# Kernel optimization log

Measured on AMD Instinct MI355X. Metric: run time of the kernel, lower is better.

The kernel has to match this reference:

```python
import jax, jax.numpy as jnp
import numpy as np

N, E, G = 50000, 500000, 512
IN_C, HID, EXTRA = 6, 32, 4
EPS = 1e-5


def setup_inputs() -> dict:
    key = jax.random.key(0)
    ks = jax.random.split(key, 24)
    rn = lambda k, s, sc=0.1: jax.random.normal(k, s, jnp.float32) * sc
    return {
        "x": jax.random.normal(ks[0], (N, IN_C), jnp.float32),
        "edge_index": jax.random.randint(ks[1], (2, E), 0, N),
        "edge_attr": jax.random.normal(ks[2], (E, 5), jnp.float32),
        "batch": jnp.sort(jax.random.randint(ks[3], (N,), 0, G)),
        "graph_attr": jax.random.normal(ks[4], (G, EXTRA), jnp.float32),
        # edge MLP 1: 5 -> 32 -> IN_C*HID
        "e1_w1": rn(ks[5], (5, 32)), "e1_b1": jnp.zeros((32,), jnp.float32),
        "e1_w2": rn(ks[6], (32, IN_C * HID)), "e1_b2": jnp.zeros((IN_C * HID,), jnp.float32),
        "root1": rn(ks[7], (IN_C, HID)), "bias1": jnp.zeros((HID,), jnp.float32),
        "bn1_g": jnp.ones((HID,), jnp.float32), "bn1_b": jnp.zeros((HID,), jnp.float32),
        # edge MLP 2: 5 -> 32 -> HID*HID
        "e2_w1": rn(ks[8], (5, 32)), "e2_b1": jnp.zeros((32,), jnp.float32),
        "e2_w2": rn(ks[9], (32, HID * HID)), "e2_b2": jnp.zeros((HID * HID,), jnp.float32),
        "root2": rn(ks[10], (HID, HID)), "bias2": jnp.zeros((HID,), jnp.float32),
        "bn2_g": jnp.ones((HID,), jnp.float32), "bn2_b": jnp.zeros((HID,), jnp.float32),
        "fc_w": rn(ks[11], (HID + EXTRA, 3)), "fc_b": jnp.zeros((3,), jnp.float32),
    }


def _nnconv(x, src, dst, edge_attr, w1, b1, w2, b2, root, bias, in_c, out_c):
    # per-edge weight matrix from edge MLP
    h = jax.nn.relu(edge_attr @ w1 + b1)                    # [E, 32]
    W = (h @ w2 + b2).reshape(-1, in_c, out_c)              # [E, in_c, out_c]
    msg = jnp.einsum('ei,eio->eo', x[src], W)               # per-edge matvec
    agg = jax.ops.segment_sum(msg, dst, num_segments=N)
    cnt = jax.ops.segment_sum(jnp.ones((msg.shape[0],), msg.dtype), dst, num_segments=N)
    agg = agg / jnp.maximum(cnt, 1.0)[:, None]              # scatter-mean
    return agg + x @ root + bias


def _bn(x, g, b):
    mu = jnp.mean(x, axis=0)
    var = jnp.mean(jnp.square(x - mu), axis=0)
    return (x - mu) * jax.lax.rsqrt(var + EPS) * g + b


def reference(x, edge_index, edge_attr, batch, graph_attr,
              e1_w1, e1_b1, e1_w2, e1_b2, root1, bias1, bn1_g, bn1_b,
              e2_w1, e2_b1, e2_w2, e2_b2, root2, bias2, bn2_g, bn2_b,
              fc_w, fc_b):
    src, dst = edge_index[0], edge_index[1]
    h = _nnconv(x, src, dst, edge_attr, e1_w1, e1_b1, e1_w2, e1_b2, root1, bias1, IN_C, HID)
    h = jax.nn.relu(_bn(h, bn1_g, bn1_b))  # dropout = identity (eval)
    h = _nnconv(h, src, dst, edge_attr, e2_w1, e2_b1, e2_w2, e2_b2, root2, bias2, HID, HID)
    h = jax.nn.relu(_bn(h, bn2_g, bn2_b))
    # global mean pool over graphs
    psum = jax.ops.segment_sum(h, batch, num_segments=G)
    pcnt = jax.ops.segment_sum(jnp.ones((N,), h.dtype), batch, num_segments=G)
    pooled = psum / jnp.maximum(pcnt, 1.0)[:, None]
    combined = jnp.concatenate([pooled, graph_attr], axis=1)  # [G, HID+EXTRA]
    return combined @ fc_w + fc_b                              # [G, 3]
```

## Files before the change

### kernel.cpp

```cpp
#include <hip/hip_runtime.h>

#define NN 50000
#define EE 500000
#define GG 512

typedef _Float16 f16x8 __attribute__((ext_vector_type(8)));
typedef _Float16 f16x2 __attribute__((ext_vector_type(2)));
typedef float f32x16 __attribute__((ext_vector_type(16)));

union F16x8U { f16x8 v8; f16x2 v2[4]; unsigned u[4]; };

__device__ __forceinline__ unsigned splat_h(float a){
  return __builtin_bit_cast(unsigned, __builtin_amdgcn_cvt_pkrtz(a, a));
}

__device__ __forceinline__ void gload16(const _Float16* g, _Float16* l){
  __builtin_amdgcn_global_load_lds(
      (const __attribute__((address_space(1))) unsigned int*)g,
      (__attribute__((address_space(3))) unsigned int*)l, 16, 0, 0);
}

#define NL1 (20*512)
#define NL2 (72*512)
__launch_bounds__(256)
__global__ void prep_k(const float* __restrict__ x,
                       const float* __restrict__ w2a, const float* __restrict__ b2a,
                       const float* __restrict__ w2b, const float* __restrict__ b2b,
                       _Float16* __restrict__ xh, _Float16* __restrict__ BtL1,
                       _Float16* __restrict__ BtL2)
{
  int idx = blockIdx.x*256 + threadIdx.x;
  if (idx < NL1){
    int t = idx >> 9, r = idx & 511;
    int lane = r >> 3, j = r & 7;
    int col = lane & 31, hi = lane >> 5;
    int ki = 16*t + 8*hi + j;
    int k = ki >> 3, i = ki & 7;
    float v = 0.f;
    if (i < 6){
      if (k < 32)       v = w2a[k*192 + i*32 + col];
      else if (k == 32) v = b2a[i*32 + col];
    }
    BtL1[idx] = (_Float16)v;
  } else if (idx < NL1 + NL2){
    int q = idx - NL1;
    int t = q >> 9, r = q & 511;
    int lane = r >> 3, j = r & 7;
    int col = lane & 31, hi = lane >> 5;
    int ki = 16*t + 8*hi + j;
    int k = ki >> 5, i = ki & 31;
    float v = 0.f;
    if (k < 32)       v = w2b[k*1024 + i*32 + col];
    else if (k == 32) v = b2b[i*32 + col];
    BtL2[q] = (_Float16)v;
  } else {
    int j = idx - (NL1 + NL2);
    if (j < NN*8){
      int n = j >> 3, i = j & 7;
      xh[j] = (_Float16)((i < 6) ? x[n*6 + i] : 0.f);
    }
  }
}

__launch_bounds__(256)
__global__ void hist_k(const int* __restrict__ ei, int* __restrict__ hist)
{
  int e = blockIdx.x*256 + threadIdx.x;
  if (e < EE) atomicAdd(&hist[ei[EE + e]], 1);
}

__launch_bounds__(256)
__global__ void scan1_k(const int* __restrict__ hist, int* __restrict__ part,
                        int* __restrict__ blk)
{
  __shared__ int s[256];
  int t = threadIdx.x, b = blockIdx.x, i = b*256 + t;
  int v = (i < NN) ? hist[i] : 0;
  s[t] = v; __syncthreads();
  #pragma unroll
  for (int off = 1; off < 256; off <<= 1){
    int u = (t >= off) ? s[t-off] : 0;
    __syncthreads();
    s[t] += u;
    __syncthreads();
  }
  if (i < NN) part[i] = s[t] - v;
  if (t == 255) blk[b] = s[255];
}

__launch_bounds__(256)
__global__ void scan2_k(int* __restrict__ blk, int nblk)
{
  __shared__ int s[256];
  int t = threadIdx.x;
  int v = (t < nblk) ? blk[t] : 0;
  s[t] = v; __syncthreads();
  #pragma unroll
  for (int off = 1; off < 256; off <<= 1){
    int u = (t >= off) ? s[t-off] : 0;
    __syncthreads();
    s[t] += u;
    __syncthreads();
  }
  if (t < nblk) blk[t] = s[t] - v;
}

__launch_bounds__(256)
__global__ void rowptr_k(const int* __restrict__ part, const int* __restrict__ blk,
                         int* __restrict__ rowptr)
{
  int n = blockIdx.x*256 + threadIdx.x;
  if (n < NN) rowptr[n] = part[n] + blk[n >> 8];
}

__launch_bounds__(256)
__global__ void scatter_k(const int* __restrict__ ei, const float* __restrict__ ea,
                          const int* __restrict__ rowptr, int* __restrict__ cursor,
                          int* __restrict__ esrc, int* __restrict__ edst,
                          float* __restrict__ eap)
{
  int e = blockIdx.x*256 + threadIdx.x;
  if (e < EE){
    int d = ei[EE + e];
    int slot = rowptr[d] + atomicAdd(&cursor[d], 1);
    esrc[slot] = ei[e];
    edst[slot] = d;
    #pragma unroll
    for (int q = 0; q < 5; ++q) eap[(long)slot*5 + q] = ea[(long)e*5 + q];
  }
}

template<int CONV>
__launch_bounds__(512, 4)
__global__ void conv_msg_k(const _Float16* __restrict__ xh,
                           const int* __restrict__ esrc,
                           const int* __restrict__ edst,
                           const float* __restrict__ eap,
                           const float* __restrict__ w1,
                           const float* __restrict__ b1,
                           const _Float16* __restrict__ Btg,
                           const int* __restrict__ rowptr,
                           const int* __restrict__ deg,
                           float* __restrict__ agg)
{
  constexpr int BTB_F16 = (CONV == 1) ? 10240 : 8192;
  __shared__ unsigned hs2[256][37];
  __shared__ _Float16 btb[BTB_F16];
  __shared__ int segrow[258];
  __shared__ int segcnt[4];

  const int tid  = threadIdx.x;
  const int lane = tid & 63;
  const int wave = tid >> 6;
  const int e0   = blockIdx.x * 256;
  const int nvalid = (EE - e0 < 256) ? (EE - e0) : 256;

  if (CONV == 1){
    #pragma unroll
    for (int i = 0; i < 3; ++i){
      int s = wave + 8*i;
      if (s < 20) gload16(Btg + (long)s*512 + lane*8, btb + s*512);
    }
  } else {
    gload16(Btg + (long)wave*512 + lane*8, btb + wave*512);
  }

  {
    int e  = tid >> 1;
    int kb = (tid & 1) * 16;
    int eg = e0 + e;
    bool valid = eg < EE;
    float eav[5];
    #pragma unroll
    for (int q = 0; q < 5; ++q) eav[q] = valid ? eap[(long)eg*5 + q] : 0.f;
    #pragma unroll
    for (int k = kb; k < kb + 16; ++k){
      float a = b1[k];
      #pragma unroll
      for (int q = 0; q < 5; ++q) a += eav[q] * w1[q*32 + k];
      hs2[e][k] = splat_h(fmaxf(a, 0.f));
    }
    if (kb == 16){
      hs2[e][32] = splat_h(1.f);
      hs2[e][33] = 0u; hs2[e][34] = 0u; hs2[e][35] = 0u;
    }
  }
  __syncthreads();

  const int col = lane & 31;
  const int hi  = lane >> 5;
  const int el  = wave*32 + col;
  const int emy = e0 + el;
  const int src = (emy < EE) ? esrc[emy] : 0;

  F16x8U xa, xb;
  if (CONV == 1){
    xa.v8 = *(const f16x8*)(xh + (long)src*8);
    xb.v8 = xa.v8;
  } else {
    xa.v8 = *(const f16x8*)(xh + (long)src*32 + 8*hi);
    xb.v8 = *(const f16x8*)(xh + (long)src*32 + 16 + 8*hi);
  }

  unsigned h2[(CONV == 1) ? 17 : 33];
  if (CONV == 1){
    #pragma unroll
    for (int t = 0; t < 17; ++t) h2[t] = hs2[el][2*t + hi];
  } else {
    #pragma unroll
    for (int kk = 0; kk < 33; ++kk) h2[kk] = hs2[el][kk];
  }

  f32x16 acc;
  #pragma unroll
  for (int r = 0; r < 16; ++r) acc[r] = 0.f;

  if (CONV == 1){
    #pragma unroll
    for (int t = 0; t < 17; ++t){
      f16x8 bf = *(const f16x8*)&btb[t*512 + lane*8];
      f16x2 hv = __builtin_bit_cast(f16x2, h2[t]);
      F16x8U af;
      #pragma unroll
      for (int p = 0; p < 4; ++p) af.v2[p] = hv * xa.v2[p];
      acc = __builtin_amdgcn_mfma_f32_32x32x16_f16(af.v8, bf, acc, 0, 0, 0);
    }
    __syncthreads();
  } else {
    #pragma unroll
    for (int c = 0; c < 9; ++c){
      if (c < 8){
        gload16(Btg + (long)((c+1)*8 + wave)*512 + lane*8,
                btb + ((c+1)&1)*4096 + wave*512);
      }
      const int tmax = (c == 8) ? 2 : 8;
      #pragma unroll
      for (int tt = 0; tt < tmax; ++tt){
        const int t = c*8 + tt;
        f16x8 bf = *(const f16x8*)&btb[(c&1)*4096 + tt*512 + lane*8];
        f16x2 hv = __builtin_bit_cast(f16x2, h2[t >> 1]);
        const F16x8U& xs = (t & 1) ? xb : xa;
        F16x8U af;
        #pragma unroll
        for (int p = 0; p < 4; ++p) af.v2[p] = hv * xs.v2[p];
        acc = __builtin_amdgcn_mfma_f32_32x32x16_f16(af.v8, bf, acc, 0, 0, 0);
      }
      __syncthreads();
    }
  }

  float* msg = (float*)&hs2[0][0];

  #pragma unroll
  for (int g = 0; g < 4; ++g){
    #pragma unroll
    for (int r = 0; r < 4; ++r){
      int row = wave*32 + r + 8*g + 4*hi;
      msg[row*37 + col] = acc[4*g + r];
    }
  }

  bool st = false;
  if (tid < 256){
    int eg = e0 + tid;
    st = (tid < nvalid) && (tid == 0 || edst[eg] != edst[eg-1]);
  }
  unsigned long long m = __ballot(st);
  int rank = __popcll(m & ((1ull << lane) - 1ull));
  if (tid < 256 && lane == 0) segcnt[wave] = (int)__popcll(m);
  __syncthreads();
  int nseg = segcnt[0] + segcnt[1] + segcnt[2] + segcnt[3];
  if (st){
    int off = 0;
    #pragma unroll
    for (int w = 0; w < 3; ++w) if (w < wave) off += segcnt[w];
    segrow[rank + off] = tid;
  }
  if (tid == 256) segrow[nseg] = nvalid;
  __syncthreads();

  const int c2 = tid & 31;
  for (int s = tid >> 5; s < nseg; s += 16){
    int r0 = segrow[s], r1 = segrow[s+1];
    float sum = 0.f;
    for (int r = r0; r < r1; ++r) sum += msg[r*37 + c2];
    int d  = edst[e0 + r0];
    int rp = rowptr[d];
    if (rp >= e0 && rp + deg[d] <= e0 + nvalid)
      agg[(long)d*32 + c2] = sum;
    else
      atomicAdd(&agg[(long)d*32 + c2], sum);
  }
}

template<int IN_C>
__launch_bounds__(256)
__global__ void node_update_k(const float* __restrict__ xin, const float* __restrict__ root,
                              const float* __restrict__ bias, const int* __restrict__ cnt,
                              float* __restrict__ buf, float* __restrict__ stats, int N)
{
  __shared__ float rs[IN_C*32];
  __shared__ float bs[32];
  __shared__ float redS[4][32], redQ[4][32];
  int tid = threadIdx.x;
  for (int i = tid; i < IN_C*32; i += 256) rs[i] = root[i];
  if (tid < 32) bs[tid] = bias[tid];
  __syncthreads();
  int o = tid & 31, slot = tid >> 5;
  float s = 0.f, q = 0.f;
  for (int n = blockIdx.x*8 + slot; n < N; n += gridDim.x*8){
    float c = fmaxf((float)cnt[n], 1.f);
    float v = buf[(long)n*32 + o] / c + bs[o];
    if constexpr (IN_C == 32){
      const float4* xr = (const float4*)&xin[(long)n*32];
      #pragma unroll
      for (int i4 = 0; i4 < 8; ++i4){
        float4 xv = xr[i4];
        v += xv.x*rs[(i4*4+0)*32+o] + xv.y*rs[(i4*4+1)*32+o]
           + xv.z*rs[(i4*4+2)*32+o] + xv.w*rs[(i4*4+3)*32+o];
      }
    } else {
      const float2* xr = (const float2*)&xin[(long)n*6];
      #pragma unroll
      for (int i2 = 0; i2 < 3; ++i2){
        float2 xv = xr[i2];
        v += xv.x*rs[(i2*2+0)*32+o] + xv.y*rs[(i2*2+1)*32+o];
      }
    }
    buf[(long)n*32 + o] = v;
    s += v; q += v*v;
  }
  s += __shfl_xor(s, 32); q += __shfl_xor(q, 32);
  int wv = tid >> 6;
  if ((tid & 63) < 32){ redS[wv][o] = s; redQ[wv][o] = q; }
  __syncthreads();
  if (tid < 32){
    float ts = 0.f, tq = 0.f;
    #pragma unroll
    for (int w = 0; w < 4; ++w){ ts += redS[w][tid]; tq += redQ[w][tid]; }
    atomicAdd(&stats[tid], ts); atomicAdd(&stats[32 + tid], tq);
  }
}

__launch_bounds__(256)
__global__ void bn_relu_k(float* __restrict__ buf, _Float16* __restrict__ bufh,
                          const float* __restrict__ stats,
                          const float* __restrict__ gg, const float* __restrict__ bb,
                          float invN, int total)
{
  int i = blockIdx.x*256 + threadIdx.x;
  if (i < total){
    int o = i & 31;
    float mu  = stats[o] * invN;
    float var = stats[32+o] * invN - mu*mu;
    float v = fmaxf((buf[i] - mu) * rsqrtf(var + 1e-5f) * gg[o] + bb[o], 0.f);
    buf[i]  = v;
    bufh[i] = (_Float16)v;
  }
}

__launch_bounds__(256)
__global__ void bn_pool_k(const float* __restrict__ buf, const float* __restrict__ stats,
                          const float* __restrict__ gg, const float* __restrict__ bb,
                          const int* __restrict__ batch, float* __restrict__ psum,
                          float* __restrict__ pcnt, float invN, int N)
{
  constexpr int NPB  = 512;
  constexpr int MAXG = 33;
  __shared__ float gsum[MAXG][33];
  int tid = threadIdx.x;
  int n0  = blockIdx.x * NPB;
  for (int i = tid; i < MAXG*33; i += 256) (&gsum[0][0])[i] = 0.f;
  __syncthreads();

  int o = tid & 31, slot = tid >> 5;
  int gfirst = batch[n0];
  float mu  = stats[o] * invN;
  float var = stats[32+o] * invN - mu*mu;
  float sc  = rsqrtf(var + 1e-5f) * gg[o];
  float sh  = bb[o] - mu*sc;
  int nend  = (N - n0 < NPB) ? N : n0 + NPB;

  float acc = 0.f, cacc = 0.f;
  int curls = -1;
  for (int n = n0 + slot; n < nend; n += 8){
    int ls = batch[n] - gfirst;
    float v = fmaxf(buf[(long)n*32 + o]*sc + sh, 0.f);
    if (ls != curls){
      if (curls >= 0){
        if ((unsigned)curls < MAXG){
          if (acc  != 0.f) atomicAdd(&gsum[curls][o], acc);
          if (o == 0 && cacc != 0.f) atomicAdd(&gsum[curls][32], cacc);
        } else {
          if (acc  != 0.f) atomicAdd(&psum[(long)(gfirst+curls)*32 + o], acc);
          if (o == 0 && cacc != 0.f) atomicAdd(&pcnt[gfirst+curls], cacc);
        }
      }
      acc = 0.f; cacc = 0.f; curls = ls;
    }
    acc += v;
    if (o == 0) cacc += 1.f;
  }
  if (curls >= 0){
    if ((unsigned)curls < MAXG){
      if (acc  != 0.f) atomicAdd(&gsum[curls][o], acc);
      if (o == 0 && cacc != 0.f) atomicAdd(&gsum[curls][32], cacc);
    } else {
      if (acc  != 0.f) atomicAdd(&psum[(long)(gfirst+curls)*32 + o], acc);
      if (o == 0 && cacc != 0.f) atomicAdd(&pcnt[gfirst+curls], cacc);
    }
  }
  __syncthreads();

  for (int i = tid; i < MAXG*32; i += 256){
    int ls = i >> 5, c = i & 31;
    float v = gsum[ls][c];
    if (v != 0.f) atomicAdd(&psum[(long)(gfirst+ls)*32 + c], v);
  }
  if (tid < MAXG){
    float v = gsum[tid][32];
    if (v != 0.f) atomicAdd(&pcnt[gfirst + tid], v);
  }
}

__launch_bounds__(256)
__global__ void final_k(const float* __restrict__ psum, const float* __restrict__ pcnt,
                        const float* __restrict__ gattr, const float* __restrict__ fcw,
                        const float* __restrict__ fcb, float* __restrict__ out, int G)
{
  int g = blockIdx.x*256 + threadIdx.x;
  if (g < G){
    float c = fmaxf(pcnt[g], 1.f);
    float o0 = fcb[0], o1 = fcb[1], o2 = fcb[2];
    #pragma unroll
    for (int j = 0; j < 32; ++j){
      float p = psum[g*32+j] / c;
      o0 += p*fcw[j*3+0]; o1 += p*fcw[j*3+1]; o2 += p*fcw[j*3+2];
    }
    #pragma unroll
    for (int j = 0; j < 4; ++j){
      float a = gattr[g*4+j];
      o0 += a*fcw[(32+j)*3+0]; o1 += a*fcw[(32+j)*3+1]; o2 += a*fcw[(32+j)*3+2];
    }
    out[g*3+0] = o0; out[g*3+1] = o1; out[g*3+2] = o2;
  }
}

extern "C" void kernel_launch(void* const* d_in, const int* in_sizes, int n_in,
                              void* d_out, int out_size, void* d_ws, size_t ws_size,
                              hipStream_t stream)
{
  const float* x     = (const float*)d_in[0];
  const int*   ei    = (const int*)  d_in[1];
  const float* ea    = (const float*)d_in[2];
  const int*   batch = (const int*)  d_in[3];
  const float* gattr = (const float*)d_in[4];
  const float* e1_w1 = (const float*)d_in[5];
  const float* e1_b1 = (const float*)d_in[6];
  const float* e1_w2 = (const float*)d_in[7];
  const float* e1_b2 = (const float*)d_in[8];
  const float* root1 = (const float*)d_in[9];
  const float* bias1 = (const float*)d_in[10];
  const float* bn1_g = (const float*)d_in[11];
  const float* bn1_b = (const float*)d_in[12];
  const float* e2_w1 = (const float*)d_in[13];
  const float* e2_b1 = (const float*)d_in[14];
  const float* e2_w2 = (const float*)d_in[15];
  const float* e2_b2 = (const float*)d_in[16];
  const float* root2 = (const float*)d_in[17];
  const float* bias2 = (const float*)d_in[18];
  const float* bn2_g = (const float*)d_in[19];
  const float* bn2_b = (const float*)d_in[20];
  const float* fc_w  = (const float*)d_in[21];
  const float* fc_b  = (const float*)d_in[22];
  float* out = (float*)d_out;

  float* ws = (float*)d_ws;
  const long NM = (long)NN*32;
  const int NBLK = (NN + 255) / 256;

  float* bufA   = ws;
  float* bufB   = bufA + NM;
  float* stats  = bufB + NM;
  float* psum   = stats + 128;
  float* pcnt   = psum + GG*32;
  int*   hist   = (int*)(pcnt + GG);
  int*   cursor = hist + NN;
  long zero_elems = 2*NM + 128 + GG*32 + GG + 2L*NN;
  int*   part   = cursor + NN;
  int*   blk    = part + NN;
  int*   rowptr = blk + 256;
  int*   esrc   = rowptr + NN;
  int*   edst   = esrc + EE;
  float* eap    = (float*)(edst + EE);
  _Float16* bufAh = (_Float16*)(eap + (long)EE*5);
  _Float16* xh    = bufAh + NM;
  _Float16* BtL1  = xh + (long)NN*8;
  _Float16* BtL2  = BtL1 + NL1;

  (void)hipMemsetAsync(d_ws, 0, (size_t)zero_elems * 4, stream);

  const int PREP_ELEMS = NL1 + NL2 + NN*8;
  prep_k<<<(PREP_ELEMS + 255)/256, 256, 0, stream>>>(x, e1_w2, e1_b2, e2_w2, e2_b2,
                                                     xh, BtL1, BtL2);

  const int EGRID = (EE + 255)/256;
  hist_k<<<EGRID, 256, 0, stream>>>(ei, hist);
  scan1_k<<<NBLK, 256, 0, stream>>>(hist, part, blk);
  scan2_k<<<1, 256, 0, stream>>>(blk, NBLK);
  rowptr_k<<<NBLK, 256, 0, stream>>>(part, blk, rowptr);
  scatter_k<<<EGRID, 256, 0, stream>>>(ei, ea, rowptr, cursor, esrc, edst, eap);

  const int EBLK = (EE + 255) / 256;
  conv_msg_k<1><<<EBLK, 512, 0, stream>>>(xh, esrc, edst, eap, e1_w1, e1_b1, BtL1,
                                          rowptr, hist, bufA);
  node_update_k<6><<<512, 256, 0, stream>>>(x, root1, bias1, hist, bufA, stats, NN);
  bn_relu_k<<<(int)((NM + 255)/256), 256, 0, stream>>>(bufA, bufAh, stats, bn1_g, bn1_b,
                                                       1.f/NN, (int)NM);
  conv_msg_k<2><<<EBLK, 512, 0, stream>>>(bufAh, esrc, edst, eap, e2_w1, e2_b1, BtL2,
                                          rowptr, hist, bufB);
  node_update_k<32><<<512, 256, 0, stream>>>(bufA, root2, bias2, hist, bufB, stats + 64, NN);
  bn_pool_k<<<(NN + 511)/512, 256, 0, stream>>>(bufB, stats + 64, bn2_g, bn2_b, batch,
                                                psum, pcnt, 1.f/NN, NN);
  final_k<<<2, 256, 0, stream>>>(psum, pcnt, gattr, fc_w, fc_b, out, GG);
}
```

Baseline: 321.0 us.

## Store edge permutation instead of permuted attrs; split MFMA accumulators

The scatter kernel now writes only a permutation index and destination instead of copying source indices and 5-float edge attributes into sorted order. Both conv kernels gather edge attributes and source indices through the permutation. This removes the permuted-copy write traffic but adds indirect, uncoalesced reads in each conv. The MFMA chain is also split into two independent accumulators to shorten the dependency chain, and the conv1 B-tile load is trimmed to the 17 tiles actually used.

```diff
diff --git a/kernel.cpp b/kernel.cpp
--- a/kernel.cpp
+++ b/kernel.cpp
@@ -114,28 +114,26 @@
 }
 
 __launch_bounds__(256)
-__global__ void scatter_k(const int* __restrict__ ei, const float* __restrict__ ea,
-                          const int* __restrict__ rowptr, int* __restrict__ cursor,
-                          int* __restrict__ esrc, int* __restrict__ edst,
-                          float* __restrict__ eap)
+__global__ void scatter_k(const int* __restrict__ ei, const int* __restrict__ rowptr,
+                          int* __restrict__ cursor,
+                          int* __restrict__ perm, int* __restrict__ edst)
 {
   int e = blockIdx.x*256 + threadIdx.x;
   if (e < EE){
     int d = ei[EE + e];
     int slot = rowptr[d] + atomicAdd(&cursor[d], 1);
-    esrc[slot] = ei[e];
+    perm[slot] = e;
     edst[slot] = d;
-    #pragma unroll
-    for (int q = 0; q < 5; ++q) eap[(long)slot*5 + q] = ea[(long)e*5 + q];
   }
 }
 
 template<int CONV>
 __launch_bounds__(512, 4)
 __global__ void conv_msg_k(const _Float16* __restrict__ xh,
-                           const int* __restrict__ esrc,
+                           const int* __restrict__ perm,
                            const int* __restrict__ edst,
-                           const float* __restrict__ eap,
+                           const int* __restrict__ ei,
+                           const float* __restrict__ ea,
                            const float* __restrict__ w1,
                            const float* __restrict__ b1,
                            const _Float16* __restrict__ Btg,
@@ -159,7 +157,7 @@
     #pragma unroll
     for (int i = 0; i < 3; ++i){
       int s = wave + 8*i;
-      if (s < 20) gload16(Btg + (long)s*512 + lane*8, btb + s*512);
+      if (s < 17) gload16(Btg + (long)s*512 + lane*8, btb + s*512);
     }
   } else {
     gload16(Btg + (long)wave*512 + lane*8, btb + wave*512);
@@ -170,9 +168,10 @@
     int kb = (tid & 1) * 16;
     int eg = e0 + e;
     bool valid = eg < EE;
+    int oe = valid ? perm[eg] : 0;
     float eav[5];
     #pragma unroll
-    for (int q = 0; q < 5; ++q) eav[q] = valid ? eap[(long)eg*5 + q] : 0.f;
+    for (int q = 0; q < 5; ++q) eav[q] = valid ? ea[(long)oe*5 + q] : 0.f;
     #pragma unroll
     for (int k = kb; k < kb + 16; ++k){
       float a = b1[k];
@@ -191,7 +190,7 @@
   const int hi  = lane >> 5;
   const int el  = wave*32 + col;
   const int emy = e0 + el;
-  const int src = (emy < EE) ? esrc[emy] : 0;
+  const int src = (emy < EE) ? ei[perm[emy]] : 0;
 
   F16x8U xa, xb;
   if (CONV == 1){
@@ -211,9 +210,9 @@
     for (int kk = 0; kk < 33; ++kk) h2[kk] = hs2[el][kk];
   }
 
-  f32x16 acc;
+  f32x16 ac0, ac1;
   #pragma unroll
-  for (int r = 0; r < 16; ++r) acc[r] = 0.f;
+  for (int r = 0; r < 16; ++r){ ac0[r] = 0.f; ac1[r] = 0.f; }
 
   if (CONV == 1){
     #pragma unroll
@@ -223,7 +222,8 @@
       F16x8U af;
       #pragma unroll
       for (int p = 0; p < 4; ++p) af.v2[p] = hv * xa.v2[p];
-      acc = __builtin_amdgcn_mfma_f32_32x32x16_f16(af.v8, bf, acc, 0, 0, 0);
+      if (t & 1) ac1 = __builtin_amdgcn_mfma_f32_32x32x16_f16(af.v8, bf, ac1, 0, 0, 0);
+      else       ac0 = __builtin_amdgcn_mfma_f32_32x32x16_f16(af.v8, bf, ac0, 0, 0, 0);
     }
     __syncthreads();
   } else {
@@ -243,11 +243,16 @@
         F16x8U af;
         #pragma unroll
         for (int p = 0; p < 4; ++p) af.v2[p] = hv * xs.v2[p];
-        acc = __builtin_amdgcn_mfma_f32_32x32x16_f16(af.v8, bf, acc, 0, 0, 0);
+        if (tt & 1) ac1 = __builtin_amdgcn_mfma_f32_32x32x16_f16(af.v8, bf, ac1, 0, 0, 0);
+        else        ac0 = __builtin_amdgcn_mfma_f32_32x32x16_f16(af.v8, bf, ac0, 0, 0, 0);
       }
       __syncthreads();
     }
   }
+
+  f32x16 acc;
+  #pragma unroll
+  for (int r = 0; r < 16; ++r) acc[r] = ac0[r] + ac1[r];
 
   float* msg = (float*)&hs2[0][0];
 
@@ -490,10 +495,9 @@
   int*   part   = cursor + NN;
   int*   blk    = part + NN;
   int*   rowptr = blk + 256;
-  int*   esrc   = rowptr + NN;
-  int*   edst   = esrc + EE;
-  float* eap    = (float*)(edst + EE);
-  _Float16* bufAh = (_Float16*)(eap + (long)EE*5);
+  int*   perm   = rowptr + NN;
+  int*   edst   = perm + EE;
+  _Float16* bufAh = (_Float16*)(edst + EE);
   _Float16* xh    = bufAh + NM;
   _Float16* BtL1  = xh + (long)NN*8;
   _Float16* BtL2  = BtL1 + NL1;
@@ -509,15 +513,15 @@
   scan1_k<<<NBLK, 256, 0, stream>>>(hist, part, blk);
   scan2_k<<<1, 256, 0, stream>>>(blk, NBLK);
   rowptr_k<<<NBLK, 256, 0, stream>>>(part, blk, rowptr);
-  scatter_k<<<EGRID, 256, 0, stream>>>(ei, ea, rowptr, cursor, esrc, edst, eap);
+  scatter_k<<<EGRID, 256, 0, stream>>>(ei, rowptr, cursor, perm, edst);
 
   const int EBLK = (EE + 255) / 256;
-  conv_msg_k<1><<<EBLK, 512, 0, stream>>>(xh, esrc, edst, eap, e1_w1, e1_b1, BtL1,
+  conv_msg_k<1><<<EBLK, 512, 0, stream>>>(xh, perm, edst, ei, ea, e1_w1, e1_b1, BtL1,
                                           rowptr, hist, bufA);
   node_update_k<6><<<512, 256, 0, stream>>>(x, root1, bias1, hist, bufA, stats, NN);
   bn_relu_k<<<(int)((NM + 255)/256), 256, 0, stream>>>(bufA, bufAh, stats, bn1_g, bn1_b,
                                                        1.f/NN, (int)NM);
-  conv_msg_k<2><<<EBLK, 512, 0, stream>>>(bufAh, esrc, edst, eap, e2_w1, e2_b1, BtL2,
+  conv_msg_k<2><<<EBLK, 512, 0, stream>>>(bufAh, perm, edst, ei, ea, e2_w1, e2_b1, BtL2,
                                           rowptr, hist, bufB);
   node_update_k<32><<<512, 256, 0, stream>>>(bufA, root2, bias2, hist, bufB, stats + 64, NN);
   bn_pool_k<<<(NN + 511)/512, 256, 0, stream>>>(bufB, stats + 64, bn2_g, bn2_b, batch,
```

After: 340.0 us. 1.06x slower.
